# Optimization experiments

Measured on AMD Instinct MI355X. Metric: run time of the kernel, lower is better.

## Reference

```python
import jax, jax.numpy as jnp
import numpy as np

# dims (match init_kwargs / input_specs)
B, T = 32, 512
DIM, DEPTH, HEADS, NB_FEAT, N_MASKS = 256, 6, 8, 128, 4
DIM_HEAD = DIM // HEADS  # 32
FF_MULT = 4
KERNEL_EPS = 1e-4


def _orth_proj(key, m, d):
    # FAVOR+ gaussian orthogonal random features: stacked QR blocks, row norms from fresh gaussians
    nb = m // d
    keys = jax.random.split(key, nb + 1)
    blocks = []
    for i in range(nb):
        g = jax.random.normal(keys[i], (d, d))
        q, _ = jnp.linalg.qr(g)
        blocks.append(q.T)
    proj = jnp.concatenate(blocks, axis=0)  # (m, d)
    norms = jnp.linalg.norm(jax.random.normal(keys[-1], (m, d)), axis=-1)
    return (proj * norms[:, None]).astype(jnp.float32)


def setup_inputs() -> dict:
    key = jax.random.key(0)
    ks = jax.random.split(key, 12)
    init = lambda k, sh: (jax.random.normal(k, sh, dtype=jnp.float32) * 0.02)
    L = DEPTH
    return {
        "mel": jax.random.normal(ks[0], (B, DIM, T), dtype=jnp.float32),
        "proj": _orth_proj(ks[1], NB_FEAT, DIM_HEAD),
        "ln1_g": jnp.ones((L, DIM), jnp.float32), "ln1_b": jnp.zeros((L, DIM), jnp.float32),
        "Wq": init(ks[2], (L, DIM, DIM)), "Wk": init(ks[3], (L, DIM, DIM)),
        "Wv": init(ks[4], (L, DIM, DIM)),
        "Wo": init(ks[5], (L, DIM, DIM)), "bo": jnp.zeros((L, DIM), jnp.float32),
        "ln2_g": jnp.ones((L, DIM), jnp.float32), "ln2_b": jnp.zeros((L, DIM), jnp.float32),
        "W1": init(ks[6], (L, DIM, FF_MULT * DIM)), "b1": jnp.zeros((L, FF_MULT * DIM), jnp.float32),
        "W2": init(ks[7], (L, FF_MULT * DIM, DIM)), "b2": jnp.zeros((L, DIM), jnp.float32),
        "Wm": init(ks[8], (DIM, N_MASKS)), "bm": jnp.zeros((N_MASKS,), jnp.float32),
    }


def _ln(x, g, b):
    mu = jnp.mean(x, -1, keepdims=True)
    var = jnp.var(x, -1, keepdims=True)
    return (x - mu) * jax.lax.rsqrt(var + 1e-5) * g + b


def _softmax_kernel(x, proj, is_query):
    # x: (B,H,N,dh), proj: (m,dh)
    dn = x.shape[-1] ** -0.25
    ratio = proj.shape[0] ** -0.5
    xd = jnp.einsum('bhnd,md->bhnm', x * dn, proj)
    diag = 0.5 * jnp.sum(jnp.square(x * dn), axis=-1, keepdims=True)
    if is_query:
        mx = jnp.max(xd, axis=-1, keepdims=True)
    else:
        mx = jnp.max(xd, axis=(-1, -2), keepdims=True)
    return ratio * (jnp.exp(xd - diag - mx) + KERNEL_EPS)


def _split_heads(x):
    b, n, _ = x.shape
    return x.reshape(b, n, HEADS, DIM_HEAD).transpose(0, 2, 1, 3)  # (B,H,N,dh)


def _forward(mel, proj, ln1_g, ln1_b, Wq, Wk, Wv, Wo, bo, ln2_g, ln2_b, W1, b1, W2, b2, Wm, bm):
    x = jnp.transpose(mel, (0, 2, 1))  # (B, T, DIM)
    for l in range(DEPTH):
        # --- FAVOR+ self-attention (pre-LN, non-causal linear attention) ---
        h = _ln(x, ln1_g[l], ln1_b[l])
        q = _split_heads(h @ Wq[l])
        k = _split_heads(h @ Wk[l])
        v = _split_heads(h @ Wv[l])
        qp = _softmax_kernel(q, proj, True)   # (B,H,T,m)
        kp = _softmax_kernel(k, proj, False)  # (B,H,T,m)
        ctx = jnp.einsum('bhnm,bhnd->bhmd', kp, v)          # (B,H,m,dh)
        o = jnp.einsum('bhnm,bhmd->bhnd', qp, ctx)          # (B,H,T,dh)
        denom = jnp.einsum('bhnm,bhm->bhn', qp, kp.sum(axis=2))
        o = o / denom[..., None]
        o = o.transpose(0, 2, 1, 3).reshape(x.shape[0], x.shape[1], DIM)
        x = x + o @ Wo[l] + bo[l]
        h = _ln(x, ln2_g[l], ln2_b[l])
        x = x + jax.nn.gelu(h @ W1[l] + b1[l]) @ W2[l] + b2[l]
    masks = x @ Wm + bm                  # (B, T, M)
    return jnp.transpose(masks, (0, 2, 1))  # (B, M, T)


def reference(mel, proj, ln1_g, ln1_b, Wq, Wk, Wv, Wo, bo, ln2_g, ln2_b, W1, b1, W2, b2, Wm, bm):
    return _forward(mel, proj, ln1_g, ln1_b, Wq, Wk, Wv, Wo, bo, ln2_g, ln2_b, W1, b1, W2, b2, Wm, bm)
```

## Files before the change

kernel.cpp:

```cpp
#include <hip/hip_runtime.h>
#include <math.h>

#define B 32
#define T 512
#define D 256
#define H 8
#define DH 32
#define MF 128
#define NLAYER 6
#define FF 1024
#define NM 4
#define BT (B*T)
#define BH (B*H)

#define DN2H 0.08838834764831845f
#define DNS  0.4204482076268573f
#define RATIO 0.08838834764831845f
#define KEPS 1e-4f

typedef __attribute__((ext_vector_type(8))) short short8;
typedef __attribute__((ext_vector_type(4))) float f32x4;

#define MFMA(a, b, c) __builtin_amdgcn_mfma_f32_16x16x32_bf16(a, b, c, 0, 0, 0)

#define SWZG(l) (((((l) & 3) + (((l) >> 3) & 3)) & 3) * 8)
#define RS(li, gi) (((((gi) - ((li) >> 1)) & 3)) * 8)

__device__ __forceinline__ ushort f2b(float x) {
  union { float f; unsigned u; } c; c.f = x;
  unsigned r = (c.u + 0x7FFFu + ((c.u >> 16) & 1u)) >> 16;
  return (ushort)r;
}
__device__ __forceinline__ float bf2f(ushort u) {
  union { unsigned u; float f; } c; c.u = ((unsigned)u) << 16;
  return c.f;
}
__device__ __forceinline__ void gload16(const ushort* g, ushort* l) {
  __builtin_amdgcn_global_load_lds((const __attribute__((address_space(1))) void*)g,
                                   (__attribute__((address_space(3))) void*)l, 16, 0, 0);
}

__global__ void transpose_mel(const float* __restrict__ mel, float* __restrict__ x) {
  __shared__ float tile[32][33];
  int b = blockIdx.z;
  int d0 = blockIdx.y * 32, t0 = blockIdx.x * 32;
  int tx = threadIdx.x, ty = threadIdx.y;
  #pragma unroll
  for (int i = 0; i < 32; i += 8)
    tile[ty + i][tx] = mel[(b * D + d0 + ty + i) * T + t0 + tx];
  __syncthreads();
  #pragma unroll
  for (int i = 0; i < 32; i += 8)
    x[(b * T + t0 + ty + i) * D + d0 + tx] = tile[tx][ty + i];
}

__global__ void wtrans(const float* __restrict__ W, ushort* __restrict__ WT,
                       int K, int N, size_t lin, size_t lout) {
  __shared__ float tile[32][33];
  int l = blockIdx.z;
  const float* Wl = W + (size_t)l * lin;
  ushort* WTl = WT + (size_t)l * lout;
  int k0 = blockIdx.y * 32, n0 = blockIdx.x * 32;
  int tx = threadIdx.x, ty = threadIdx.y;
  #pragma unroll
  for (int i = 0; i < 32; i += 8)
    tile[ty + i][tx] = Wl[(size_t)(k0 + ty + i) * N + n0 + tx];
  __syncthreads();
  #pragma unroll
  for (int i = 0; i < 32; i += 8)
    WTl[(size_t)(n0 + ty + i) * K + k0 + tx] = f2b(tile[tx][ty + i]);
}

__global__ void proj_conv(const float* __restrict__ proj, ushort* __restrict__ projd) {
  int e = blockIdx.x * 256 + threadIdx.x;
  if (e < MF * DH) projd[e] = f2b(proj[e] * DNS);
}

__global__ __launch_bounds__(256) void ln_kernel(const float* __restrict__ x, const float* __restrict__ g,
                          const float* __restrict__ bb, ushort* __restrict__ y) {
  int row = blockIdx.x * 4 + (threadIdx.x >> 6);
  int lane = threadIdx.x & 63;
  const float4 v = ((const float4*)(x + (size_t)row * D))[lane];
  float s = v.x + v.y + v.z + v.w;
  #pragma unroll
  for (int off = 32; off; off >>= 1) s += __shfl_down(s, off);
  s = __shfl(s, 0);
  float mu = s * (1.0f / 256.0f);
  float dx = v.x - mu, dy = v.y - mu, dz = v.z - mu, dw = v.w - mu;
  float q = dx * dx + dy * dy + dz * dz + dw * dw;
  #pragma unroll
  for (int off = 32; off; off >>= 1) q += __shfl_down(q, off);
  q = __shfl(q, 0);
  float rstd = rsqrtf(q * (1.0f / 256.0f) + 1e-5f);
  const float4 gg = ((const float4*)g)[lane];
  const float4 be = ((const float4*)bb)[lane];
  ushort4 o;
  o.x = f2b(dx * rstd * gg.x + be.x);
  o.y = f2b(dy * rstd * gg.y + be.y);
  o.z = f2b(dz * rstd * gg.z + be.z);
  o.w = f2b(dw * rstd * gg.w + be.w);
  ((ushort4*)(y + (size_t)row * D))[lane] = o;
}

template<int EPI, int BM>
__global__ __launch_bounds__(256) void gemm_bf16(
    const ushort* __restrict__ A, const ushort* __restrict__ BTm,
    const float* __restrict__ bias,
    ushort* __restrict__ outB,
    ushort* __restrict__ qo, ushort* __restrict__ ko, ushort* __restrict__ vT,
    int N, int K) {
  constexpr int MFR = BM / 32;
  __shared__ __align__(16) ushort Al[BM * 32];
  __shared__ __align__(16) ushort Bl[128 * 32];
  int tid = threadIdx.x;
  int wave = tid >> 6, lane = tid & 63;
  int wr = wave >> 1, wc = wave & 1;
  int gi = lane >> 4, li = lane & 15;
  int lrow = lane >> 2, lkb = SWZG(lane);
  int row0 = blockIdx.y * BM, col0 = blockIdx.x * 128;
  f32x4 acc[MFR][4] = {};
  for (int k0 = 0; k0 < K; k0 += 32) {
    #pragma unroll
    for (int i = 0; i < BM / 64; i++) {
      int chunk = wave * (BM / 64) + i;
      int row = chunk * 16 + lrow;
      gload16(&A[(size_t)(row0 + row) * K + k0 + lkb], &Al[chunk * 512]);
    }
    #pragma unroll
    for (int i = 0; i < 2; i++) {
      int chunk = wave * 2 + i;
      int row = chunk * 16 + lrow;
      gload16(&BTm[(size_t)(col0 + row) * K + k0 + lkb], &Bl[chunk * 512]);
    }
    __syncthreads();
    short8 a[MFR], b[4];
    #pragma unroll
    for (int m = 0; m < MFR; m++)
      a[m] = *(const short8*)&Al[(wr * (MFR * 16) + m * 16 + li) * 32 + RS(li, gi)];
    #pragma unroll
    for (int n = 0; n < 4; n++)
      b[n] = *(const short8*)&Bl[(wc * 64 + n * 16 + li) * 32 + RS(li, gi)];
    #pragma unroll
    for (int m = 0; m < MFR; m++)
      #pragma unroll
      for (int n = 0; n < 4; n++)
        acc[m][n] = MFMA(a[m], b[n], acc[m][n]);
    __syncthreads();
  }
  #pragma unroll
  for (int m = 0; m < MFR; m++) {
    int rbase = row0 + wr * (MFR * 16) + m * 16 + gi * 4;
    #pragma unroll
    for (int n = 0; n < 4; n++) {
      int col = col0 + wc * 64 + n * 16 + li;
      f32x4 v = acc[m][n];
      if (EPI == 2) {
        float bs = bias[col];
        #pragma unroll
        for (int r = 0; r < 4; r++) {
          float u = v[r] + bs;
          float p = u + 0.044715f * u * u * u;
          float gel = u / (1.0f + __expf(-1.5957691216057308f * p));
          outB[(size_t)(rbase + r) * N + col] = f2b(gel);
        }
      } else {
        if (col < 256) {
          #pragma unroll
          for (int r = 0; r < 4; r++) qo[(size_t)(rbase + r) * 256 + col] = f2b(v[r]);
        } else if (col < 512) {
          #pragma unroll
          for (int r = 0; r < 4; r++) ko[(size_t)(rbase + r) * 256 + col - 256] = f2b(v[r]);
        } else {
          int b_ = rbase >> 9, t = rbase & 511;
          int hh = (col - 512) >> 5, d = (col - 512) & 31;
          ushort4 pk;
          pk.x = f2b(v[0]); pk.y = f2b(v[1]); pk.z = f2b(v[2]); pk.w = f2b(v[3]);
          *(ushort4*)&vT[((size_t)((b_ * 8 + hh) * 32 + d)) * 512 + t] = pk;
        }
      }
    }
  }
}

__global__ __launch_bounds__(256) void ctx_fused(
    const ushort* __restrict__ kb, const ushort* __restrict__ projd,
    const ushort* __restrict__ vT, ushort* __restrict__ Bmat) {
  __shared__ __align__(16) ushort Kl[512 * 32];
  __shared__ __align__(16) ushort Pl[128 * 32];
  __shared__ __align__(16) ushort Sl[2][128 * 40];
  __shared__ __align__(16) ushort Bvl[2][32 * 32];
  __shared__ float dg_s[512];
  __shared__ float red_s[256];
  int bh = blockIdx.x;
  int b = bh >> 3, h = bh & 7;
  int tid = threadIdx.x, wave = tid >> 6, lane = tid & 63;
  int gi = lane >> 4, li = lane & 15;
  int lrow = lane >> 2, lkb = (lane & 3) * 8;
  const ushort* Kg = kb + (size_t)(b * 512) * 256 + h * 32;
  const ushort* Vg = vT + (size_t)bh * 32 * 512;
  #pragma unroll
  for (int i = 0; i < 8; i++) {
    int chunk = wave * 8 + i;
    gload16(&Kg[(size_t)(chunk * 16 + lrow) * 256 + lkb], &Kl[chunk * 512]);
  }
  #pragma unroll
  for (int i = 0; i < 2; i++) {
    int chunk = wave * 2 + i;
    gload16(&projd[(chunk * 16 + lrow) * 32 + lkb], &Pl[chunk * 512]);
  }
  __syncthreads();
  #pragma unroll
  for (int i = 0; i < 2; i++) {
    int t = tid * 2 + i;
    const ushort* kr = &Kl[t * 32];
    float s = 0.f;
    #pragma unroll
    for (int j = 0; j < 32; j++) { float v = bf2f(kr[j]); s += v * v; }
    dg_s[t] = DN2H * s;
  }
  short8 bp0 = *(const short8*)&Pl[(wave * 32 + li) * 32 + gi * 8];
  short8 bp1 = *(const short8*)&Pl[(wave * 32 + 16 + li) * 32 + gi * 8];
  float smax = -1e30f;
  for (int c = 0; c < 16; c++) {
    int t0c = c * 32;
    short8 a0 = *(const short8*)&Kl[(t0c + li) * 32 + gi * 8];
    short8 a1 = *(const short8*)&Kl[(t0c + 16 + li) * 32 + gi * 8];
    f32x4 s00 = {}, s01 = {}, s10 = {}, s11 = {};
    s00 = MFMA(a0, bp0, s00); s01 = MFMA(a0, bp1, s01);
    s10 = MFMA(a1, bp0, s10); s11 = MFMA(a1, bp1, s11);
    #pragma unroll
    for (int r = 0; r < 4; r++)
      smax = fmaxf(smax, fmaxf(fmaxf(s00[r], s01[r]), fmaxf(s10[r], s11[r])));
  }
  red_s[tid] = smax;
  __syncthreads();
  for (int s = 128; s; s >>= 1) {
    if (tid < s) red_s[tid] = fmaxf(red_s[tid], red_s[tid + s]);
    __syncthreads();
  }
  float km = red_s[0];
  f32x4 cacc[2][2] = {};
  float ks0 = 0.f, ks1 = 0.f;
  int cur = 0;
  for (int c = 0; c < 16; c++, cur ^= 1) {
    int t0c = c * 32;
    if (wave < 2)
      gload16(&Vg[(size_t)(wave * 16 + lrow) * 512 + t0c + lkb], &Bvl[cur][wave * 512]);
    short8 a0 = *(const short8*)&Kl[(t0c + li) * 32 + gi * 8];
    short8 a1 = *(const short8*)&Kl[(t0c + 16 + li) * 32 + gi * 8];
    f32x4 s00 = {}, s01 = {}, s10 = {}, s11 = {};
    s00 = MFMA(a0, bp0, s00); s01 = MFMA(a0, bp1, s01);
    s10 = MFMA(a1, bp0, s10); s11 = MFMA(a1, bp1, s11);
    ushort4 w00, w01, w10, w11;
    #pragma unroll
    for (int r = 0; r < 4; r++) {
      float d0 = dg_s[t0c + gi * 4 + r];
      float d1 = dg_s[t0c + 16 + gi * 4 + r];
      float k00 = RATIO * (__expf(s00[r] - d0 - km) + KEPS);
      float k01 = RATIO * (__expf(s01[r] - d0 - km) + KEPS);
      float k10 = RATIO * (__expf(s10[r] - d1 - km) + KEPS);
      float k11 = RATIO * (__expf(s11[r] - d1 - km) + KEPS);
      ks0 += k00 + k10; ks1 += k01 + k11;
      ((ushort*)&w00)[r] = f2b(k00); ((ushort*)&w01)[r] = f2b(k01);
      ((ushort*)&w10)[r] = f2b(k10); ((ushort*)&w11)[r] = f2b(k11);
    }
    *(ushort4*)&Sl[cur][(wave * 32 + li) * 40 + gi * 4]           = w00;
    *(ushort4*)&Sl[cur][(wave * 32 + 16 + li) * 40 + gi * 4]      = w01;
    *(ushort4*)&Sl[cur][(wave * 32 + li) * 40 + 16 + gi * 4]      = w10;
    *(ushort4*)&Sl[cur][(wave * 32 + 16 + li) * 40 + 16 + gi * 4] = w11;
    __syncthreads();
    short8 ca0 = *(const short8*)&Sl[cur][(wave * 32 + li) * 40 + gi * 8];
    short8 ca1 = *(const short8*)&Sl[cur][(wave * 32 + 16 + li) * 40 + gi * 8];
    short8 cb0 = *(const short8*)&Bvl[cur][li * 32 + gi * 8];
    short8 cb1 = *(const short8*)&Bvl[cur][(16 + li) * 32 + gi * 8];
    cacc[0][0] = MFMA(ca0, cb0, cacc[0][0]);
    cacc[0][1] = MFMA(ca0, cb1, cacc[0][1]);
    cacc[1][0] = MFMA(ca1, cb0, cacc[1][0]);
    cacc[1][1] = MFMA(ca1, cb1, cacc[1][1]);
  }
  ks0 += __shfl_xor(ks0, 16); ks0 += __shfl_xor(ks0, 32);
  ks1 += __shfl_xor(ks1, 16); ks1 += __shfl_xor(ks1, 32);
  if (gi == 0) {
    Bmat[((size_t)bh * 48 + 32) * 128 + wave * 32 + li] = f2b(ks0);
    Bmat[((size_t)bh * 48 + 32) * 128 + wave * 32 + 16 + li] = f2b(ks1);
  }
  #pragma unroll
  for (int m = 0; m < 2; m++)
    #pragma unroll
    for (int n = 0; n < 2; n++) {
      int dd = n * 16 + li;
      int mg = wave * 32 + m * 16 + gi * 4;
      ushort4 pk;
      pk.x = f2b(cacc[m][n][0]); pk.y = f2b(cacc[m][n][1]);
      pk.z = f2b(cacc[m][n][2]); pk.w = f2b(cacc[m][n][3]);
      *(ushort4*)&Bmat[((size_t)bh * 48 + dd) * 128 + mg] = pk;
    }
  for (int e = tid; e < 15 * 128; e += 256)
    Bmat[((size_t)bh * 48 + 33) * 128 + e] = 0;
}

__global__ __launch_bounds__(256) void favq_o(
    const ushort* __restrict__ qb, const ushort* __restrict__ projd,
    const ushort* __restrict__ Bmat, ushort* __restrict__ ob) {
  __shared__ __align__(16) ushort Ql[64 * 32];
  __shared__ __align__(16) ushort Pl[128 * 32];
  __shared__ __align__(16) ushort Sl[64 * 136];
  __shared__ __align__(16) ushort Bml[48 * 136];
  __shared__ float dgq[64];
  int bh = blockIdx.y;
  int t0 = blockIdx.x * 64;
  int b = bh >> 3, h = bh & 7;
  int tid = threadIdx.x, wave = tid >> 6, lane = tid & 63;
  int gi = lane >> 4, li = lane & 15;
  int lrow = lane >> 2, lkb = (lane & 3) * 8;
  const ushort* Qg = qb + (size_t)(b * 512) * 256 + h * 32;
  gload16(&Qg[(size_t)(t0 + wave * 16 + lrow) * 256 + lkb], &Ql[wave * 512]);
  #pragma unroll
  for (int i = 0; i < 2; i++) {
    int chunk = wave * 2 + i;
    gload16(&projd[(chunk * 16 + lrow) * 32 + lkb], &Pl[chunk * 512]);
  }
  #pragma unroll
  for (int j = 0; j < 3; j++) {
    int c = j * 256 + tid;
    int r = c >> 4, g = c & 15;
    *(uint4*)&Bml[r * 136 + g * 8] = *(const uint4*)&Bmat[(size_t)bh * 48 * 128 + r * 128 + g * 8];
  }
  __syncthreads();
  if (tid < 64) {
    const ushort* qr = &Ql[tid * 32];
    float s = 0.f;
    #pragma unroll
    for (int j = 0; j < 32; j++) { float v = bf2f(qr[j]); s += v * v; }
    dgq[tid] = DN2H * s;
  }
  short8 bq = *(const short8*)&Ql[(wave * 16 + li) * 32 + gi * 8];
  f32x4 sacc[8] = {};
  #pragma unroll
  for (int m = 0; m < 8; m++) {
    short8 a = *(const short8*)&Pl[(m * 16 + li) * 32 + gi * 8];
    sacc[m] = MFMA(a, bq, sacc[m]);
  }
  __syncthreads();
  float mx = -1e30f;
  #pragma unroll
  for (int m = 0; m < 8; m++)
    #pragma unroll
    for (int r = 0; r < 4; r++) mx = fmaxf(mx, sacc[m][r]);
  mx = fmaxf(mx, __shfl_xor(mx, 16));
  mx = fmaxf(mx, __shfl_xor(mx, 32));
  float dg = dgq[wave * 16 + li];
  #pragma unroll
  for (int m = 0; m < 8; m++) {
    ushort4 o4;
    #pragma unroll
    for (int r = 0; r < 4; r++)
      ((ushort*)&o4)[r] = f2b(RATIO * (__expf(sacc[m][r] - dg - mx) + KEPS));
    *(ushort4*)&Sl[(wave * 16 + li) * 136 + m * 16 + gi * 4] = o4;
  }
  __syncthreads();
  f32x4 oacc[3] = {};
  #pragma unroll
  for (int ks = 0; ks < 4; ks++) {
    short8 a = *(const short8*)&Sl[(wave * 16 + li) * 136 + ks * 32 + gi * 8];
    #pragma unroll
    for (int n = 0; n < 3; n++) {
      short8 bb = *(const short8*)&Bml[(n * 16 + li) * 136 + ks * 32 + gi * 8];
      oacc[n] = MFMA(a, bb, oacc[n]);
    }
  }
  int t = t0 + wave * 16 + gi * 4;
  float den[4];
  #pragma unroll
  for (int r = 0; r < 4; r++) den[r] = __shfl(oacc[2][r], lane & 48);
  #pragma unroll
  for (int n = 0; n < 2; n++)
    #pragma unroll
    for (int r = 0; r < 4; r++)
      ob[((size_t)(b * 512) + t + r) * 256 + h * 32 + n * 16 + li] = f2b(oacc[n][r] / den[r]);
}

template<int MODE>
__global__ __launch_bounds__(256) void gemm_ln2(
    const ushort* __restrict__ A, const ushort* __restrict__ BTm,
    const float* __restrict__ bias, const float* __restrict__ res,
    float* __restrict__ x, const float* __restrict__ g, const float* __restrict__ bvec,
    ushort* __restrict__ hout,
    const float* __restrict__ Wm, const float* __restrict__ bm, float* __restrict__ mout,
    int K) {
  __shared__ __align__(16) ushort Al[64 * 32];
  __shared__ __align__(16) ushort Bl[256 * 32];
  __shared__ float rs1[4 * 64];
  __shared__ float rs2[4 * 64];
  __shared__ float pmS[4 * 256];
  int tid = threadIdx.x, wave = tid >> 6, lane = tid & 63;
  int gi = lane >> 4, li = lane & 15;
  int lrow = lane >> 2, lkb = SWZG(lane);
  int row0 = blockIdx.x * 64;
  int wc = wave;
  f32x4 acc[4][4] = {};
  for (int k0 = 0; k0 < K; k0 += 32) {
    gload16(&A[(size_t)(row0 + wave * 16 + lrow) * K + k0 + lkb], &Al[wave * 512]);
    #pragma unroll
    for (int i = 0; i < 4; i++) {
      int chunk = wave * 4 + i;
      gload16(&BTm[(size_t)(chunk * 16 + lrow) * K + k0 + lkb], &Bl[chunk * 512]);
    }
    __syncthreads();
    short8 a[4], b[4];
    #pragma unroll
    for (int m = 0; m < 4; m++)
      a[m] = *(const short8*)&Al[(m * 16 + li) * 32 + RS(li, gi)];
    #pragma unroll
    for (int n = 0; n < 4; n++)
      b[n] = *(const short8*)&Bl[(wc * 64 + n * 16 + li) * 32 + RS(li, gi)];
    #pragma unroll
    for (int m = 0; m < 4; m++)
      #pragma unroll
      for (int n = 0; n < 4; n++)
        acc[m][n] = MFMA(a[m], b[n], acc[m][n]);
    __syncthreads();
  }
  #pragma unroll
  for (int m = 0; m < 4; m++) {
    #pragma unroll
    for (int r = 0; r < 4; r++) {
      int row = row0 + m * 16 + gi * 4 + r;
      int ridx = m * 16 + gi * 4 + r;
      float s1 = 0.f, s2 = 0.f;
      #pragma unroll
      for (int n = 0; n < 4; n++) {
        int col = wc * 64 + n * 16 + li;
        float val = acc[m][n][r] + bias[col] + res[(size_t)row * 256 + col];
        acc[m][n][r] = val;
        s1 += val; s2 += val * val;
      }
      if (MODE == 0) {
        #pragma unroll
        for (int off = 1; off <= 8; off <<= 1) { s1 += __shfl_xor(s1, off); s2 += __shfl_xor(s2, off); }
        if (li == 0) { rs1[wave * 64 + ridx] = s1; rs2[wave * 64 + ridx] = s2; }
      } else {
        #pragma unroll
        for (int msk = 0; msk < NM; msk++) {
          float sm = 0.f;
          #pragma unroll
          for (int n = 0; n < 4; n++) {
            int col = wc * 64 + n * 16 + li;
            sm += acc[m][n][r] * Wm[col * NM + msk];
          }
          #pragma unroll
          for (int off = 1; off <= 8; off <<= 1) sm += __shfl_xor(sm, off);
          if (li == 0) pmS[wave * 256 + ridx * 4 + msk] = sm;
        }
      }
    }
  }
  __syncthreads();
  if (MODE == 0) {
    float g4[4], bv4[4];
    #pragma unroll
    for (int n = 0; n < 4; n++) {
      int col = wc * 64 + n * 16 + li;
      g4[n] = g[col]; bv4[n] = bvec[col];
    }
    #pragma unroll
    for (int m = 0; m < 4; m++) {
      #pragma unroll
      for (int r = 0; r < 4; r++) {
        int row = row0 + m * 16 + gi * 4 + r;
        int ridx = m * 16 + gi * 4 + r;
        float t1 = rs1[ridx] + rs1[64 + ridx] + rs1[128 + ridx] + rs1[192 + ridx];
        float t2 = rs2[ridx] + rs2[64 + ridx] + rs2[128 + ridx] + rs2[192 + ridx];
        float mu = t1 * (1.f / 256.f);
        float rstd = rsqrtf(t2 * (1.f / 256.f) - mu * mu + 1e-5f);
        #pragma unroll
        for (int n = 0; n < 4; n++) {
          int col = wc * 64 + n * 16 + li;
          float val = acc[m][n][r];
          x[(size_t)row * 256 + col] = val;
          hout[(size_t)row * 256 + col] = f2b((val - mu) * rstd * g4[n] + bv4[n]);
        }
      }
    }
  } else {
    int ridx = tid >> 2, msk = tid & 3;
    float tot = pmS[ridx * 4 + msk] + pmS[256 + ridx * 4 + msk] +
                pmS[512 + ridx * 4 + msk] + pmS[768 + ridx * 4 + msk];
    int grow = row0 + ridx;
    int bb_ = grow >> 9, t = grow & 511;
    mout[((size_t)(bb_ * NM) + msk) * 512 + t] = tot + bm[msk];
  }
}

extern "C" void kernel_launch(void* const* d_in, const int* in_sizes, int n_in,
                              void* d_out, int out_size, void* d_ws, size_t ws_size,
                              hipStream_t stream) {
  const float* mel   = (const float*)d_in[0];
  const float* proj  = (const float*)d_in[1];
  const float* ln1_g = (const float*)d_in[2];
  const float* ln1_b = (const float*)d_in[3];
  const float* Wq    = (const float*)d_in[4];
  const float* Wk    = (const float*)d_in[5];
  const float* Wv    = (const float*)d_in[6];
  const float* Wo    = (const float*)d_in[7];
  const float* bo    = (const float*)d_in[8];
  const float* ln2_g = (const float*)d_in[9];
  const float* ln2_b = (const float*)d_in[10];
  const float* W1    = (const float*)d_in[11];
  const float* b1    = (const float*)d_in[12];
  const float* W2    = (const float*)d_in[13];
  const float* b2    = (const float*)d_in[14];
  const float* Wm    = (const float*)d_in[15];
  const float* bm    = (const float*)d_in[16];

  float* x      = (float*)d_ws;
  ushort* us    = (ushort*)(x + (size_t)BT * D);
  ushort* h     = us;                   us += (size_t)BT * D;
  ushort* qb    = us;                   us += (size_t)BT * D;
  ushort* kb    = us;                   us += (size_t)BT * D;
  ushort* vT    = us;                   us += (size_t)BH * 32 * T;
  ushort* ob    = us;                   us += (size_t)BT * D;
  ushort* ffh   = us;                   us += (size_t)BT * FF;
  ushort* Bmat  = us;                   us += (size_t)BH * 48 * MF;
  ushort* qkvT  = us;                   us += (size_t)NLAYER * 768 * 256;
  ushort* woT   = us;                   us += (size_t)NLAYER * 256 * 256;
  ushort* w1T   = us;                   us += (size_t)NLAYER * 1024 * 256;
  ushort* w2T   = us;                   us += (size_t)NLAYER * 256 * 1024;
  ushort* projd = us;                   us += (size_t)MF * DH;

  wtrans<<<dim3(8, 8, NLAYER), dim3(32, 8), 0, stream>>>(Wq, qkvT, 256, 256, 65536, 768 * 256);
  wtrans<<<dim3(8, 8, NLAYER), dim3(32, 8), 0, stream>>>(Wk, qkvT + 256 * 256, 256, 256, 65536, 768 * 256);
  wtrans<<<dim3(8, 8, NLAYER), dim3(32, 8), 0, stream>>>(Wv, qkvT + 512 * 256, 256, 256, 65536, 768 * 256);
  wtrans<<<dim3(8, 8, NLAYER), dim3(32, 8), 0, stream>>>(Wo, woT, 256, 256, 65536, 65536);
  wtrans<<<dim3(32, 8, NLAYER), dim3(32, 8), 0, stream>>>(W1, w1T, 256, 1024, 262144, 262144);
  wtrans<<<dim3(8, 32, NLAYER), dim3(32, 8), 0, stream>>>(W2, w2T, 1024, 256, 262144, 262144);
  proj_conv<<<16, 256, 0, stream>>>(proj, projd);

  transpose_mel<<<dim3(T / 32, D / 32, B), dim3(32, 8), 0, stream>>>(mel, x);
  ln_kernel<<<BT / 4, 256, 0, stream>>>(x, ln1_g, ln1_b, h);

  for (int l = 0; l < NLAYER; l++) {
    gemm_bf16<0, 128><<<dim3(6, 128), 256, 0, stream>>>(h, qkvT + (size_t)l * 768 * 256,
        nullptr, nullptr, qb, kb, vT, 768, 256);
    ctx_fused<<<BH, 256, 0, stream>>>(kb, projd, vT, Bmat);
    favq_o<<<dim3(8, BH), 256, 0, stream>>>(qb, projd, Bmat, ob);
    gemm_ln2<0><<<256, 256, 0, stream>>>(ob, woT + (size_t)l * 256 * 256,
        bo + l * D, x, x, ln2_g + l * D, ln2_b + l * D, h,
        nullptr, nullptr, nullptr, 256);
    gemm_bf16<2, 128><<<dim3(8, 128), 256, 0, stream>>>(h, w1T + (size_t)l * 1024 * 256,
        b1 + (size_t)l * FF, ffh, nullptr, nullptr, nullptr, 1024, 256);
    if (l < NLAYER - 1) {
      gemm_ln2<0><<<256, 256, 0, stream>>>(ffh, w2T + (size_t)l * 256 * 1024,
          b2 + l * D, x, x, ln1_g + (l + 1) * D, ln1_b + (l + 1) * D, h,
          nullptr, nullptr, nullptr, 1024);
    } else {
      gemm_ln2<1><<<256, 256, 0, stream>>>(ffh, w2T + (size_t)l * 256 * 1024,
          b2 + l * D, x, x, nullptr, nullptr, nullptr,
          Wm, bm, (float*)d_out, 1024);
    }
  }
}
```

Before: 855.6 us.

## Double-buffer LDS tiles in bf16 GEMM kernels to overlap loads with MFMA

Both the generic bf16 GEMM and the GEMM+LayerNorm kernel now keep two LDS buffers for the A and B tiles. The next K-slice is prefetched into the alternate buffer while MFMAs run on the current one. This is meant to hide global load latency and remove one barrier per iteration. In exchange it doubles LDS use for these tiles, which may lower occupancy, and correctness relies on the loads being complete before the end-of-iteration barrier.

```diff
diff --git a/kernel.cpp b/kernel.cpp
--- a/kernel.cpp
+++ b/kernel.cpp
@@ -110,8 +110,8 @@
     ushort* __restrict__ qo, ushort* __restrict__ ko, ushort* __restrict__ vT,
     int N, int K) {
   constexpr int MFR = BM / 32;
-  __shared__ __align__(16) ushort Al[BM * 32];
-  __shared__ __align__(16) ushort Bl[128 * 32];
+  __shared__ __align__(16) ushort Al[2][BM * 32];
+  __shared__ __align__(16) ushort Bl[2][128 * 32];
   int tid = threadIdx.x;
   int wave = tid >> 6, lane = tid & 63;
   int wr = wave >> 1, wc = wave & 1;
@@ -119,27 +119,32 @@
   int lrow = lane >> 2, lkb = SWZG(lane);
   int row0 = blockIdx.y * BM, col0 = blockIdx.x * 128;
   f32x4 acc[MFR][4] = {};
-  for (int k0 = 0; k0 < K; k0 += 32) {
+
+  auto stage = [&](int buf, int kk) {
     #pragma unroll
     for (int i = 0; i < BM / 64; i++) {
       int chunk = wave * (BM / 64) + i;
-      int row = chunk * 16 + lrow;
-      gload16(&A[(size_t)(row0 + row) * K + k0 + lkb], &Al[chunk * 512]);
+      gload16(&A[(size_t)(row0 + chunk * 16 + lrow) * K + kk + lkb], &Al[buf][chunk * 512]);
     }
     #pragma unroll
     for (int i = 0; i < 2; i++) {
       int chunk = wave * 2 + i;
-      int row = chunk * 16 + lrow;
-      gload16(&BTm[(size_t)(col0 + row) * K + k0 + lkb], &Bl[chunk * 512]);
-    }
-    __syncthreads();
+      gload16(&BTm[(size_t)(col0 + chunk * 16 + lrow) * K + kk + lkb], &Bl[buf][chunk * 512]);
+    }
+  };
+
+  stage(0, 0);
+  __syncthreads();
+  int cur = 0;
+  for (int k0 = 0; k0 < K; k0 += 32, cur ^= 1) {
+    if (k0 + 32 < K) stage(cur ^ 1, k0 + 32);
     short8 a[MFR], b[4];
     #pragma unroll
     for (int m = 0; m < MFR; m++)
-      a[m] = *(const short8*)&Al[(wr * (MFR * 16) + m * 16 + li) * 32 + RS(li, gi)];
+      a[m] = *(const short8*)&Al[cur][(wr * (MFR * 16) + m * 16 + li) * 32 + RS(li, gi)];
     #pragma unroll
     for (int n = 0; n < 4; n++)
-      b[n] = *(const short8*)&Bl[(wc * 64 + n * 16 + li) * 32 + RS(li, gi)];
+      b[n] = *(const short8*)&Bl[cur][(wc * 64 + n * 16 + li) * 32 + RS(li, gi)];
     #pragma unroll
     for (int m = 0; m < MFR; m++)
       #pragma unroll
@@ -388,8 +393,8 @@
     ushort* __restrict__ hout,
     const float* __restrict__ Wm, const float* __restrict__ bm, float* __restrict__ mout,
     int K) {
-  __shared__ __align__(16) ushort Al[64 * 32];
-  __shared__ __align__(16) ushort Bl[256 * 32];
+  __shared__ __align__(16) ushort Al[2][64 * 32];
+  __shared__ __align__(16) ushort Bl[2][256 * 32];
   __shared__ float rs1[4 * 64];
   __shared__ float rs2[4 * 64];
   __shared__ float pmS[4 * 256];
@@ -399,21 +404,28 @@
   int row0 = blockIdx.x * 64;
   int wc = wave;
   f32x4 acc[4][4] = {};
-  for (int k0 = 0; k0 < K; k0 += 32) {
-    gload16(&A[(size_t)(row0 + wave * 16 + lrow) * K + k0 + lkb], &Al[wave * 512]);
+
+  auto stage = [&](int buf, int kk) {
+    gload16(&A[(size_t)(row0 + wave * 16 + lrow) * K + kk + lkb], &Al[buf][wave * 512]);
     #pragma unroll
     for (int i = 0; i < 4; i++) {
       int chunk = wave * 4 + i;
-      gload16(&BTm[(size_t)(chunk * 16 + lrow) * K + k0 + lkb], &Bl[chunk * 512]);
-    }
-    __syncthreads();
+      gload16(&BTm[(size_t)(chunk * 16 + lrow) * K + kk + lkb], &Bl[buf][chunk * 512]);
+    }
+  };
+
+  stage(0, 0);
+  __syncthreads();
+  int cur = 0;
+  for (int k0 = 0; k0 < K; k0 += 32, cur ^= 1) {
+    if (k0 + 32 < K) stage(cur ^ 1, k0 + 32);
     short8 a[4], b[4];
     #pragma unroll
     for (int m = 0; m < 4; m++)
-      a[m] = *(const short8*)&Al[(m * 16 + li) * 32 + RS(li, gi)];
+      a[m] = *(const short8*)&Al[cur][(m * 16 + li) * 32 + RS(li, gi)];
     #pragma unroll
     for (int n = 0; n < 4; n++)
-      b[n] = *(const short8*)&Bl[(wc * 64 + n * 16 + li) * 32 + RS(li, gi)];
+      b[n] = *(const short8*)&Bl[cur][(wc * 64 + n * 16 + li) * 32 + RS(li, gi)];
     #pragma unroll
     for (int m = 0; m < 4; m++)
       #pragma unroll
```

Measured after the change: 805.3 us. 5.9% less time.
